# Kernel tuning notes

Hardware: AMD Instinct MI355X
Metric: run time of the kernel (lower is better)

Reference implementation:

```python
import jax, jax.numpy as jnp
import numpy as np

DIM = 768
HEADS = 12
HEAD_DIM = DIM // HEADS
B, N = 4, 2048


def setup_inputs() -> dict:
    key = jax.random.key(0)
    ks = jax.random.split(key, 5)
    s = 0.02
    return {
        "x": jax.random.normal(ks[0], (B, N, DIM), dtype=jnp.float32),
        "w_qkv": jax.random.normal(ks[1], (DIM, 3 * DIM), dtype=jnp.float32) * s,
        "b_qkv": jnp.zeros((3 * DIM,), dtype=jnp.float32),
        "w_proj": jax.random.normal(ks[2], (DIM, DIM), dtype=jnp.float32) * s,
        "b_proj": jnp.zeros((DIM,), dtype=jnp.float32),
    }


def reference(x, w_qkv, b_qkv, w_proj, b_proj):
    b, n, c = x.shape
    scale = HEAD_DIM ** -0.5
    qkv = x @ w_qkv + b_qkv                       # [B,N,3C]
    qkv = qkv.reshape(b, n, 3, HEADS, HEAD_DIM)
    q = qkv[:, :, 0].transpose(0, 2, 1, 3)        # [B,H,N,D]
    k = qkv[:, :, 1].transpose(0, 2, 1, 3)
    v = qkv[:, :, 2].transpose(0, 2, 1, 3)
    attn = jnp.einsum("bhqd,bhkd->bhqk", q, k) * scale
    attn = jax.nn.softmax(attn, axis=-1)
    out = jnp.einsum("bhqk,bhkd->bhqd", attn, v)  # [B,H,N,D]
    out = out.transpose(0, 2, 1, 3).reshape(b, n, c)
    return out @ w_proj + b_proj
```

## Files before the change

kernel.cpp:

```cpp
#include <hip/hip_runtime.h>

typedef short sh8 __attribute__((ext_vector_type(8)));
typedef short sh4 __attribute__((ext_vector_type(4)));
typedef float f32x4 __attribute__((ext_vector_type(4)));
typedef float f32x16 __attribute__((ext_vector_type(16)));
typedef unsigned u32x4 __attribute__((ext_vector_type(4)));

extern "C" __device__ float __ocml_native_exp2_f32(float);

__device__ __forceinline__ short f2bf(float f) {
  unsigned u = __builtin_bit_cast(unsigned, f);
  u += 0x7fffu + ((u >> 16) & 1u);
  return (short)(u >> 16);
}

__device__ __forceinline__ void gload16(const short* g, short* l) {
  __builtin_amdgcn_global_load_lds(
      (const __attribute__((address_space(1))) unsigned*)g,
      (__attribute__((address_space(3))) unsigned*)l, 16, 0, 0);
}

__device__ __forceinline__ void wait2_barrier() {
  asm volatile("s_waitcnt vmcnt(2)" ::: "memory");
  __builtin_amdgcn_s_barrier();
  asm volatile("" ::: "memory");
}
__device__ __forceinline__ void wait0_barrier() {
  asm volatile("s_waitcnt vmcnt(0)" ::: "memory");
  __builtin_amdgcn_s_barrier();
  asm volatile("" ::: "memory");
}

__device__ __forceinline__ int xcd_swizzle(int bidl, int nwg) {
  int q = nwg >> 3, rr = nwg & 7;
  int xcd = bidl & 7, idx = bidl >> 3;
  return (xcd < rr ? xcd * (q + 1) : rr * (q + 1) + (xcd - rr) * q) + idx;
}

__global__ void cast_f32_bf16(const float* __restrict__ in, short* __restrict__ out, int n) {
  int i = (blockIdx.x * blockDim.x + threadIdx.x) * 4;
  if (i >= n) return;
  float4 f = *(const float4*)(in + i);
  sh4 o;
  o.x = f2bf(f.x); o.y = f2bf(f.y); o.z = f2bf(f.z); o.w = f2bf(f.w);
  *(sh4*)(out + i) = o;
}

__global__ __launch_bounds__(256) void transpose_cast_t(
    const float* __restrict__ in, short* __restrict__ out, int K, int Nn) {
  __shared__ short Tl[64][72];
  const int t = threadIdx.x;
  const int n0 = blockIdx.x * 64, k0 = blockIdx.y * 64;
  const int kr0 = t >> 4;
  const int nc = (t & 15) * 4;
#pragma unroll
  for (int p = 0; p < 4; p++) {
    int kr = kr0 + p * 16;
    float4 f = *(const float4*)(in + (size_t)(k0 + kr) * Nn + n0 + nc);
    Tl[nc + 0][kr] = f2bf(f.x);
    Tl[nc + 1][kr] = f2bf(f.y);
    Tl[nc + 2][kr] = f2bf(f.z);
    Tl[nc + 3][kr] = f2bf(f.w);
  }
  __syncthreads();
  const int nr0 = t >> 3;
  const int kk = (t & 7) * 8;
#pragma unroll
  for (int p = 0; p < 2; p++) {
    int nr = nr0 + p * 32;
    *(sh8*)(out + (size_t)(n0 + nr) * K + k0 + kk) = *(const sh8*)&Tl[nr][kk];
  }
}

template <int OUTF32>
__global__ __launch_bounds__(256, 4) void gemm_bt(
    const short* __restrict__ A, const short* __restrict__ Bt,
    const float* __restrict__ bias, void* __restrict__ Cv,
    int M, int Nn, int K) {
  __shared__ short SMEM[20480];
  const int t = threadIdx.x;
  const int wave = t >> 6, lane = t & 63, quad = lane >> 4, l15 = lane & 15;
  const int wm = (wave >> 1) * 64, wn = (wave & 1) * 64;
  const int nwg = gridDim.x * gridDim.y;
  const int wg = xcd_swizzle(blockIdx.y * gridDim.x + blockIdx.x, nwg);
  const int row0 = (wg / gridDim.x) * 128, col0 = (wg % gridDim.x) * 128;
  f32x4 acc[4][4] = {};

  const int srow = t >> 2;
  const int ssl = ((t & 3) ^ ((t >> 3) & 3)) * 8;
  const short* Asrc0 = A + (size_t)(row0 + srow) * K + ssl;
  const short* Asrc1 = A + (size_t)(row0 + 64 + srow) * K + ssl;
  const short* Bsrc0 = Bt + (size_t)(col0 + srow) * K + ssl;
  const short* Bsrc1 = Bt + (size_t)(col0 + 64 + srow) * K + ssl;
  short* AsF = SMEM;
  short* BsF = SMEM + 12288;
  const int wdst = wave * 512;

  const int soA = (quad ^ ((l15 >> 1) & 3)) * 8;

  const int T = K >> 5;
  gload16(Asrc0, AsF + wdst);
  gload16(Asrc1, AsF + 2048 + wdst);
  gload16(Bsrc0, BsF + wdst);
  gload16(Bsrc1, BsF + 2048 + wdst);
  gload16(Asrc0 + 32, AsF + 4096 + wdst);
  gload16(Asrc1 + 32, AsF + 4096 + 2048 + wdst);

  int ra = 0, wa = 2;
  for (int tt = 0; tt < T; tt++) {
    if (tt + 1 < T) wait2_barrier(); else wait0_barrier();
    if (tt + 1 < T) {
      const int k0 = (tt + 1) * 32;
      short* Bd = BsF + ((tt + 1) & 1) * 4096 + wdst;
      gload16(Bsrc0 + k0, Bd);
      gload16(Bsrc1 + k0, Bd + 2048);
    }
    if (tt + 2 < T) {
      const int k0 = (tt + 2) * 32;
      short* Ad = AsF + wa * 4096 + wdst;
      gload16(Asrc0 + k0, Ad);
      gload16(Asrc1 + k0, Ad + 2048);
    }
    const short* Ab = AsF + ra * 4096;
    const short* Bb = BsF + (tt & 1) * 4096;
    sh8 af[4], bfv[4];
#pragma unroll
    for (int i = 0; i < 4; i++) af[i] = *(const sh8*)&Ab[(wm + i * 16 + l15) * 32 + soA];
#pragma unroll
    for (int j = 0; j < 4; j++) bfv[j] = *(const sh8*)&Bb[(wn + j * 16 + l15) * 32 + soA];
#pragma unroll
    for (int i = 0; i < 4; i++)
#pragma unroll
      for (int j = 0; j < 4; j++)
        acc[i][j] = __builtin_amdgcn_mfma_f32_16x16x32_bf16(af[i], bfv[j], acc[i][j], 0, 0, 0);
    ra = ra == 2 ? 0 : ra + 1;
    wa = wa == 2 ? 0 : wa + 1;
  }

#pragma unroll
  for (int i = 0; i < 4; i++)
#pragma unroll
    for (int j = 0; j < 4; j++) {
      int r = row0 + wm + i * 16 + quad * 4;
      int c = col0 + wn + j * 16 + l15;
      float bv = bias[c];
#pragma unroll
      for (int e = 0; e < 4; e++) {
        float v = acc[i][j][e] + bv;
        if (OUTF32)
          ((float*)Cv)[(size_t)(r + e) * Nn + c] = v;
        else
          ((short*)Cv)[(size_t)(r + e) * Nn + c] = f2bf(v);
      }
    }
}

__global__ __launch_bounds__(256, 4) void gemm_qkv(
    const short* __restrict__ A, const short* __restrict__ Bt,
    const float* __restrict__ bias,
    short* __restrict__ Qh, short* __restrict__ Kh, short* __restrict__ VhT) {
  const int K = 768;
  __shared__ short SMEM[20480];
  const int t = threadIdx.x;
  const int wave = t >> 6, lane = t & 63, quad = lane >> 4, l15 = lane & 15;
  const int wm = (wave >> 1) * 64, wn = (wave & 1) * 64;
  const int nwg = gridDim.x * gridDim.y;
  const int wg = xcd_swizzle(blockIdx.y * gridDim.x + blockIdx.x, nwg);
  const int row0 = (wg / gridDim.x) * 128, col0 = (wg % gridDim.x) * 128;
  f32x4 acc[4][4] = {};

  const int srow = t >> 2;
  const int ssl = ((t & 3) ^ ((t >> 3) & 3)) * 8;
  const short* Asrc0 = A + (size_t)(row0 + srow) * K + ssl;
  const short* Asrc1 = A + (size_t)(row0 + 64 + srow) * K + ssl;
  const short* Bsrc0 = Bt + (size_t)(col0 + srow) * K + ssl;
  const short* Bsrc1 = Bt + (size_t)(col0 + 64 + srow) * K + ssl;
  short* AsF = SMEM;
  short* BsF = SMEM + 12288;
  const int wdst = wave * 512;

  const int soA = (quad ^ ((l15 >> 1) & 3)) * 8;

  const int T = K >> 5;
  gload16(Asrc0, AsF + wdst);
  gload16(Asrc1, AsF + 2048 + wdst);
  gload16(Bsrc0, BsF + wdst);
  gload16(Bsrc1, BsF + 2048 + wdst);
  gload16(Asrc0 + 32, AsF + 4096 + wdst);
  gload16(Asrc1 + 32, AsF + 4096 + 2048 + wdst);

  int ra = 0, wa = 2;
  for (int tt = 0; tt < T; tt++) {
    if (tt + 1 < T) wait2_barrier(); else wait0_barrier();
    if (tt + 1 < T) {
      const int k0 = (tt + 1) * 32;
      short* Bd = BsF + ((tt + 1) & 1) * 4096 + wdst;
      gload16(Bsrc0 + k0, Bd);
      gload16(Bsrc1 + k0, Bd + 2048);
    }
    if (tt + 2 < T) {
      const int k0 = (tt + 2) * 32;
      short* Ad = AsF + wa * 4096 + wdst;
      gload16(Asrc0 + k0, Ad);
      gload16(Asrc1 + k0, Ad + 2048);
    }
    const short* Ab = AsF + ra * 4096;
    const short* Bb = BsF + (tt & 1) * 4096;
    sh8 af[4], bfv[4];
#pragma unroll
    for (int i = 0; i < 4; i++) af[i] = *(const sh8*)&Ab[(wm + i * 16 + l15) * 32 + soA];
#pragma unroll
    for (int j = 0; j < 4; j++) bfv[j] = *(const sh8*)&Bb[(wn + j * 16 + l15) * 32 + soA];
#pragma unroll
    for (int i = 0; i < 4; i++)
#pragma unroll
      for (int j = 0; j < 4; j++)
        acc[i][j] = __builtin_amdgcn_mfma_f32_16x16x32_bf16(af[i], bfv[j], acc[i][j], 0, 0, 0);
    ra = ra == 2 ? 0 : ra + 1;
    wa = wa == 2 ? 0 : wa + 1;
  }

  const int s = col0 >= 1536 ? 2 : (col0 >= 768 ? 1 : 0);

  if (s < 2) {
    short* dst = s == 0 ? Qh : Kh;
    const float scl = (s == 0) ? 0.18033688011112042f : 1.0f;
#pragma unroll
    for (int j = 0; j < 4; j++) {
      int c = col0 + wn + j * 16 + l15;
      int hd = c - s * 768;
      int h = hd >> 6;
      float bv = bias[c];
#pragma unroll
      for (int i = 0; i < 4; i++) {
        int rbase = row0 + wm + i * 16 + quad * 4;
#pragma unroll
        for (int e = 0; e < 4; e++) {
          int r = rbase + e;
          int b = r >> 11, n = r & 2047;
          float v = (acc[i][j][e] + bv) * scl;
          dst[(size_t)(b * 12 + h) * 131072 + n * 64 + (hd & 63)] = f2bf(v);
        }
      }
    }
  } else {
    __syncthreads();
    short* Tl = SMEM;
#pragma unroll
    for (int j = 0; j < 4; j++) {
      int cl = wn + j * 16 + l15;
      float bv = bias[col0 + cl];
#pragma unroll
      for (int i = 0; i < 4; i++) {
        int rl = wm + i * 16 + quad * 4;
        sh4 pk;
#pragma unroll
        for (int e = 0; e < 4; e++) pk[e] = f2bf(acc[i][j][e] + bv);
        *(sh4*)&Tl[cl * 136 + rl] = pk;
      }
    }
    __syncthreads();
    const int b = row0 >> 11, n0 = row0 & 2047;
    const int h0 = (col0 - 1536) >> 6;
#pragma unroll
    for (int p = 0; p < 8; p++) {
      int cl = (t >> 4) + p * 16;
      int nn = (t & 15) * 8;
      int hg = h0 + (cl >> 6);
      int d = cl & 63;
      sh8 vv = *(const sh8*)&Tl[cl * 136 + nn];
      *(sh8*)&VhT[(size_t)(b * 12 + hg) * 131072 + (size_t)d * 2048 + n0 + nn] = vv;
    }
  }
}

__global__ __launch_bounds__(512, 4) void attn10(const short* __restrict__ Qh,
                                                 const short* __restrict__ Kh,
                                                 const short* __restrict__ VhT,
                                                 short* __restrict__ outb) {
  const int bid = blockIdx.x;
  const int qb = bid / 48;
  const int bh = bid - qb * 48;
  const int t = threadIdx.x;
  const int w = t >> 6, lane = t & 63;
  const int wl = w & 3, g = w >> 2;
  const int l31 = lane & 31, hi = lane >> 5;

  __shared__ short SM[40960];

  const size_t hb = (size_t)bh * 131072;

  sh8 qa[4];
  {
    const short* qp = Qh + hb + (size_t)(qb * 128 + wl * 32 + l31) * 64 + hi * 8;
    qa[0] = *(const sh8*)(qp);
    qa[1] = *(const sh8*)(qp + 16);
    qa[2] = *(const sh8*)(qp + 32);
    qa[3] = *(const sh8*)(qp + 48);
  }
  asm volatile("s_waitcnt vmcnt(0)" ::: "memory");

  f32x16 o[2] = {};
  f32x4 lsv = {};

  const int tg = t & 255;
  const int srow = tg >> 3;
  const int ssl = ((tg & 7) ^ (srow & 7)) * 8;
  const short* Ksrc = Kh + hb + (size_t)(g * 1024 + srow) * 64 + ssl;
  const short* Vsrc = VhT + hb + (size_t)srow * 2048 + g * 1024 + ssl;
  short* KlF = SM + g * 20480;
  short* VtF = KlF + 8192;
  const int wdst = wl * 512;

  const int sw7 = l31 & 7;
  int rsl[4];
#pragma unroll
  for (int ks = 0; ks < 4; ks++) rsl[ks] = (((ks << 1) | hi) ^ sw7) * 8;

  gload16(Ksrc, KlF + wdst);
  gload16(Ksrc + (size_t)32 * 64, KlF + 2048 + wdst);
  gload16(Vsrc, VtF + wdst);
  gload16(Vsrc + (size_t)32 * 2048, VtF + 2048 + wdst);

  sh8 pap[4] = {};
  int vw = 1;
  int vp = 2;

  for (int kt = 0; kt < 16; kt++) {
    wait2_barrier();
    if (kt + 1 < 16) {
      const int key0 = (kt + 1) * 64;
      short* Kd = KlF + ((kt + 1) & 1) * 4096 + wdst;
      gload16(Ksrc + (size_t)key0 * 64, Kd);
      gload16(Ksrc + (size_t)(key0 + 32) * 64, Kd + 2048);
      short* Vd = VtF + vw * 4096 + wdst;
      gload16(Vsrc + key0, Vd);
      gload16(Vsrc + (size_t)32 * 2048 + key0, Vd + 2048);
    }

    const short* Kb = KlF + (kt & 1) * 4096;

    unsigned u0[8], u1[8];
#pragma unroll
    for (int kb = 0; kb < 2; kb++) {
      const short* kr = Kb + (kb * 32 + l31) * 64;
      f32x16 s = {};
#pragma unroll
      for (int ks = 0; ks < 4; ks++)
        s = __builtin_amdgcn_mfma_f32_32x32x16_bf16(*(const sh8*)(kr + rsl[ks]), qa[ks], s, 0, 0, 0);
      unsigned* uu = kb ? u1 : u0;
#pragma unroll
      for (int m = 0; m < 8; m++) {
        float e0 = __ocml_native_exp2_f32(s[2 * m]);
        float e1 = __ocml_native_exp2_f32(s[2 * m + 1]);
        lsv[m & 3] += e0 + e1;
        asm("v_cvt_pk_bf16_f32 %0, %1, %2" : "=v"(uu[m]) : "v"(e0), "v"(e1));
      }
    }

    if (kt > 0) {
      const short* Vb = VtF + vp * 4096;
      __builtin_amdgcn_s_setprio(1);
#pragma unroll
      for (int db = 0; db < 2; db++) {
        const short* vr = Vb + (db * 32 + l31) * 64;
#pragma unroll
        for (int ks = 0; ks < 4; ks++)
          o[db] = __builtin_amdgcn_mfma_f32_32x32x16_bf16(pap[ks], *(const sh8*)(vr + rsl[ks]), o[db], 0, 0, 0);
      }
      __builtin_amdgcn_s_setprio(0);
    }

#pragma unroll
    for (int kb = 0; kb < 2; kb++) {
      const unsigned* uu = kb ? u1 : u0;
      unsigned y0 = (unsigned)__shfl_xor((int)(hi ? uu[0] : uu[2]), 32, 64);
      unsigned y1 = (unsigned)__shfl_xor((int)(hi ? uu[1] : uu[3]), 32, 64);
      unsigned y2 = (unsigned)__shfl_xor((int)(hi ? uu[4] : uu[6]), 32, 64);
      unsigned y3 = (unsigned)__shfl_xor((int)(hi ? uu[5] : uu[7]), 32, 64);
      unsigned w0 = hi ? y0 : uu[0];
      unsigned w1 = hi ? y1 : uu[1];
      unsigned w2 = hi ? uu[2] : y0;
      unsigned w3 = hi ? uu[3] : y1;
      unsigned w4 = hi ? y2 : uu[4];
      unsigned w5 = hi ? y3 : uu[5];
      unsigned w6 = hi ? uu[6] : y2;
      unsigned w7 = hi ? uu[7] : y3;
      u32x4 A0 = {w0, w1, w2, w3};
      u32x4 A1 = {w4, w5, w6, w7};
      pap[2 * kb] = __builtin_bit_cast(sh8, A0);
      pap[2 * kb + 1] = __builtin_bit_cast(sh8, A1);
    }

    vw = vw == 2 ? 0 : vw + 1;
    vp = vp == 2 ? 0 : vp + 1;
  }

  wait0_barrier();
  {
    const short* Vb = VtF;
#pragma unroll
    for (int db = 0; db < 2; db++) {
      const short* vr = Vb + (db * 32 + l31) * 64;
#pragma unroll
      for (int ks = 0; ks < 4; ks++)
        o[db] = __builtin_amdgcn_mfma_f32_32x32x16_bf16(pap[ks], *(const sh8*)(vr + rsl[ks]), o[db], 0, 0, 0);
    }
  }

  float ls = lsv[0] + lsv[1] + lsv[2] + lsv[3];
  ls += __shfl_xor(ls, 32, 64);

  __syncthreads();
  float* cb = (float*)SM;
  const int ci = (wl * 64 + lane) * 33;
  if (g == 1) {
#pragma unroll
    for (int r = 0; r < 16; r++) {
      cb[ci + r] = o[0][r];
      cb[ci + 16 + r] = o[1][r];
    }
    cb[ci + 32] = ls;
  }
  __syncthreads();
  if (g == 0) {
#pragma unroll
    for (int r = 0; r < 16; r++) {
      o[0][r] += cb[ci + r];
      o[1][r] += cb[ci + 16 + r];
    }
    ls += cb[ci + 32];
    float inv = 1.f / ls;

    const int b = bh / 12, hh = bh - b * 12;
#pragma unroll
    for (int r = 0; r < 16; r++) {
      int qr = (r & 3) + 8 * (r >> 2) + 4 * hi;
      float iv = __shfl(inv, qr, 64);
      int n = qb * 128 + wl * 32 + qr;
      short* op = outb + (size_t)(b * 2048 + n) * 768 + hh * 64 + l31;
      op[0] = f2bf(o[0][r] * iv);
      op[32] = f2bf(o[1][r] * iv);
    }
  }
}

extern "C" void kernel_launch(void* const* d_in, const int* in_sizes, int n_in,
                              void* d_out, int out_size, void* d_ws, size_t ws_size,
                              hipStream_t stream) {
  const float* x = (const float*)d_in[0];
  const float* w_qkv = (const float*)d_in[1];
  const float* b_qkv = (const float*)d_in[2];
  const float* w_proj = (const float*)d_in[3];
  const float* b_proj = (const float*)d_in[4];
  float* out = (float*)d_out;

  char* p = (char*)d_ws;
  short* xb = (short*)p;     p += (size_t)8192 * 768 * 2;
  short* wqkvT = (short*)p;  p += (size_t)2304 * 768 * 2;
  short* wprojT = (short*)p; p += (size_t)768 * 768 * 2;
  short* Qh = (short*)p;     p += (size_t)48 * 131072 * 2;
  short* Kh = (short*)p;     p += (size_t)48 * 131072 * 2;
  short* VhT = (short*)p;    p += (size_t)48 * 131072 * 2;
  short* attnb = (short*)p;  p += (size_t)8192 * 768 * 2;

  cast_f32_bf16<<<(8192 * 768 / 4) / 256, 256, 0, stream>>>(x, xb, 8192 * 768);
  {
    dim3 gt(2304 / 64, 768 / 64);
    transpose_cast_t<<<gt, 256, 0, stream>>>(w_qkv, wqkvT, 768, 2304);
  }
  {
    dim3 gt(768 / 64, 768 / 64);
    transpose_cast_t<<<gt, 256, 0, stream>>>(w_proj, wprojT, 768, 768);
  }

  dim3 g1(2304 / 128, 8192 / 128);
  gemm_qkv<<<g1, 256, 0, stream>>>(xb, wqkvT, b_qkv, Qh, Kh, VhT);

  attn10<<<16 * 48, 512, 0, stream>>>(Qh, Kh, VhT, attnb);

  dim3 g2(768 / 128, 8192 / 128);
  gemm_bt<1><<<g2, 256, 0, stream>>>(attnb, wprojT, b_proj, out, 8192, 768, 768);
}
```

Before: 214.5 us.

## Halve attention key tile to 32 to cut LDS and raise occupancy

The attention kernel now streams 32 keys per iteration instead of 64. That halves the K/V shared-memory staging buffers and raises the launch-bounds occupancy hint from 4 to 6 blocks. The V tile uses a new 4-way XOR swizzle matching the 32-wide rows, and the P·V step uses two MFMA k-steps instead of four. The aim is more resident waves to hide latency. In exchange the loop runs twice as many barriered iterations, each with less MFMA work, which adds sync and issue overhead. With 768 blocks on the device, the extra occupancy may not be usable.

Result: slower. 303.2 us (+41.3%).

```diff
diff --git a/kernel.cpp b/kernel.cpp
--- a/kernel.cpp
+++ b/kernel.cpp
@@ -22,6 +22,11 @@
 
 __device__ __forceinline__ void wait2_barrier() {
   asm volatile("s_waitcnt vmcnt(2)" ::: "memory");
+  __builtin_amdgcn_s_barrier();
+  asm volatile("" ::: "memory");
+}
+__device__ __forceinline__ void wait1_barrier() {
+  asm volatile("s_waitcnt vmcnt(1)" ::: "memory");
   __builtin_amdgcn_s_barrier();
   asm volatile("" ::: "memory");
 }
@@ -274,7 +279,7 @@
   }
 }
 
-__global__ __launch_bounds__(512, 4) void attn10(const short* __restrict__ Qh,
+__global__ __launch_bounds__(512, 6) void attn11(const short* __restrict__ Qh,
                                                  const short* __restrict__ Kh,
                                                  const short* __restrict__ VhT,
                                                  short* __restrict__ outb) {
@@ -286,7 +291,7 @@
   const int wl = w & 3, g = w >> 2;
   const int l31 = lane & 31, hi = lane >> 5;
 
-  __shared__ short SM[40960];
+  __shared__ short SM[20480];
 
   const size_t hb = (size_t)bh * 131072;
 
@@ -306,90 +311,85 @@
   const int tg = t & 255;
   const int srow = tg >> 3;
   const int ssl = ((tg & 7) ^ (srow & 7)) * 8;
+  const int vrow = tg >> 2;
+  const int vssl = ((tg & 3) ^ ((tg >> 3) & 3)) * 8;
   const short* Ksrc = Kh + hb + (size_t)(g * 1024 + srow) * 64 + ssl;
-  const short* Vsrc = VhT + hb + (size_t)srow * 2048 + g * 1024 + ssl;
-  short* KlF = SM + g * 20480;
-  short* VtF = KlF + 8192;
+  const short* Vsrc = VhT + hb + (size_t)vrow * 2048 + g * 1024 + vssl;
+  short* KlF = SM + g * 10240;
+  short* VtF = KlF + 4096;
   const int wdst = wl * 512;
 
   const int sw7 = l31 & 7;
-  int rsl[4];
-#pragma unroll
-  for (int ks = 0; ks < 4; ks++) rsl[ks] = (((ks << 1) | hi) ^ sw7) * 8;
+  const int swv = (l31 >> 1) & 3;
+  int rslk[4], rslv[2];
+#pragma unroll
+  for (int ks = 0; ks < 4; ks++) rslk[ks] = (((ks << 1) | hi) ^ sw7) * 8;
+#pragma unroll
+  for (int ks = 0; ks < 2; ks++) rslv[ks] = (((ks << 1) | hi) ^ swv) * 8;
 
   gload16(Ksrc, KlF + wdst);
-  gload16(Ksrc + (size_t)32 * 64, KlF + 2048 + wdst);
   gload16(Vsrc, VtF + wdst);
-  gload16(Vsrc + (size_t)32 * 2048, VtF + 2048 + wdst);
-
-  sh8 pap[4] = {};
+
+  sh8 pap[2] = {};
   int vw = 1;
   int vp = 2;
 
-  for (int kt = 0; kt < 16; kt++) {
-    wait2_barrier();
-    if (kt + 1 < 16) {
-      const int key0 = (kt + 1) * 64;
-      short* Kd = KlF + ((kt + 1) & 1) * 4096 + wdst;
-      gload16(Ksrc + (size_t)key0 * 64, Kd);
-      gload16(Ksrc + (size_t)(key0 + 32) * 64, Kd + 2048);
-      short* Vd = VtF + vw * 4096 + wdst;
-      gload16(Vsrc + key0, Vd);
-      gload16(Vsrc + (size_t)32 * 2048 + key0, Vd + 2048);
-    }
-
-    const short* Kb = KlF + (kt & 1) * 4096;
-
-    unsigned u0[8], u1[8];
-#pragma unroll
-    for (int kb = 0; kb < 2; kb++) {
-      const short* kr = Kb + (kb * 32 + l31) * 64;
+  for (int kt = 0; kt < 32; kt++) {
+    wait1_barrier();
+    if (kt + 1 < 32) {
+      const int key0 = (kt + 1) * 32;
+      gload16(Ksrc + (size_t)key0 * 64, KlF + ((kt + 1) & 1) * 2048 + wdst);
+      gload16(Vsrc + key0, VtF + vw * 2048 + wdst);
+    }
+
+    const short* Kb = KlF + (kt & 1) * 2048;
+
+    unsigned u[8];
+    {
+      const short* kr = Kb + l31 * 64;
       f32x16 s = {};
 #pragma unroll
       for (int ks = 0; ks < 4; ks++)
-        s = __builtin_amdgcn_mfma_f32_32x32x16_bf16(*(const sh8*)(kr + rsl[ks]), qa[ks], s, 0, 0, 0);
-      unsigned* uu = kb ? u1 : u0;
+        s = __builtin_amdgcn_mfma_f32_32x32x16_bf16(*(const sh8*)(kr + rslk[ks]), qa[ks], s, 0, 0, 0);
 #pragma unroll
       for (int m = 0; m < 8; m++) {
         float e0 = __ocml_native_exp2_f32(s[2 * m]);
         float e1 = __ocml_native_exp2_f32(s[2 * m + 1]);
         lsv[m & 3] += e0 + e1;
-        asm("v_cvt_pk_bf16_f32 %0, %1, %2" : "=v"(uu[m]) : "v"(e0), "v"(e1));
+        asm("v_cvt_pk_bf16_f32 %0, %1, %2" : "=v"(u[m]) : "v"(e0), "v"(e1));
       }
     }
 
     if (kt > 0) {
-      const short* Vb = VtF + vp * 4096;
+      const short* Vb = VtF + vp * 2048;
       __builtin_amdgcn_s_setprio(1);
 #pragma unroll
       for (int db = 0; db < 2; db++) {
-        const short* vr = Vb + (db * 32 + l31) * 64;
-#pragma unroll
-        for (int ks = 0; ks < 4; ks++)
-          o[db] = __builtin_amdgcn_mfma_f32_32x32x16_bf16(pap[ks], *(const sh8*)(vr + rsl[ks]), o[db], 0, 0, 0);
+        const short* vr = Vb + (db * 32 + l31) * 32;
+#pragma unroll
+        for (int ks = 0; ks < 2; ks++)
+          o[db] = __builtin_amdgcn_mfma_f32_32x32x16_bf16(pap[ks], *(const sh8*)(vr + rslv[ks]), o[db], 0, 0, 0);
       }
       __builtin_amdgcn_s_setprio(0);
     }
 
-#pragma unroll
-    for (int kb = 0; kb < 2; kb++) {
-      const unsigned* uu = kb ? u1 : u0;
-      unsigned y0 = (unsigned)__shfl_xor((int)(hi ? uu[0] : uu[2]), 32, 64);
-      unsigned y1 = (unsigned)__shfl_xor((int)(hi ? uu[1] : uu[3]), 32, 64);
-      unsigned y2 = (unsigned)__shfl_xor((int)(hi ? uu[4] : uu[6]), 32, 64);
-      unsigned y3 = (unsigned)__shfl_xor((int)(hi ? uu[5] : uu[7]), 32, 64);
-      unsigned w0 = hi ? y0 : uu[0];
-      unsigned w1 = hi ? y1 : uu[1];
-      unsigned w2 = hi ? uu[2] : y0;
-      unsigned w3 = hi ? uu[3] : y1;
-      unsigned w4 = hi ? y2 : uu[4];
-      unsigned w5 = hi ? y3 : uu[5];
-      unsigned w6 = hi ? uu[6] : y2;
-      unsigned w7 = hi ? uu[7] : y3;
+    {
+      unsigned y0 = (unsigned)__shfl_xor((int)(hi ? u[0] : u[2]), 32, 64);
+      unsigned y1 = (unsigned)__shfl_xor((int)(hi ? u[1] : u[3]), 32, 64);
+      unsigned y2 = (unsigned)__shfl_xor((int)(hi ? u[4] : u[6]), 32, 64);
+      unsigned y3 = (unsigned)__shfl_xor((int)(hi ? u[5] : u[7]), 32, 64);
+      unsigned w0 = hi ? y0 : u[0];
+      unsigned w1 = hi ? y1 : u[1];
+      unsigned w2 = hi ? u[2] : y0;
+      unsigned w3 = hi ? u[3] : y1;
+      unsigned w4 = hi ? y2 : u[4];
+      unsigned w5 = hi ? y3 : u[5];
+      unsigned w6 = hi ? u[6] : y2;
+      unsigned w7 = hi ? u[7] : y3;
       u32x4 A0 = {w0, w1, w2, w3};
       u32x4 A1 = {w4, w5, w6, w7};
-      pap[2 * kb] = __builtin_bit_cast(sh8, A0);
-      pap[2 * kb + 1] = __builtin_bit_cast(sh8, A1);
+      pap[0] = __builtin_bit_cast(sh8, A0);
+      pap[1] = __builtin_bit_cast(sh8, A1);
     }
 
     vw = vw == 2 ? 0 : vw + 1;
@@ -398,13 +398,13 @@
 
   wait0_barrier();
   {
-    const short* Vb = VtF;
+    const short* Vb = VtF + vp * 2048;
 #pragma unroll
     for (int db = 0; db < 2; db++) {
-      const short* vr = Vb + (db * 32 + l31) * 64;
-#pragma unroll
-      for (int ks = 0; ks < 4; ks++)
-        o[db] = __builtin_amdgcn_mfma_f32_32x32x16_bf16(pap[ks], *(const sh8*)(vr + rsl[ks]), o[db], 0, 0, 0);
+      const short* vr = Vb + (db * 32 + l31) * 32;
+#pragma unroll
+      for (int ks = 0; ks < 2; ks++)
+        o[db] = __builtin_amdgcn_mfma_f32_32x32x16_bf16(pap[ks], *(const sh8*)(vr + rslv[ks]), o[db], 0, 0, 0);
     }
   }
 
@@ -477,7 +477,7 @@
   dim3 g1(2304 / 128, 8192 / 128);
   gemm_qkv<<<g1, 256, 0, stream>>>(xb, wqkvT, b_qkv, Qh, Kh, VhT);
 
-  attn10<<<16 * 48, 512, 0, stream>>>(Qh, Kh, VhT, attnb);
+  attn11<<<16 * 48, 512, 0, stream>>>(Qh, Kh, VhT, attnb);
 
   dim3 g2(768 / 128, 8192 / 128);
   gemm_bt<1><<<g2, 256, 0, stream>>>(attnb, wprojT, b_proj, out, 8192, 768, 768);
```
